# Kernel optimization log

Measured on AMD Instinct MI355X. Metric: run time of the kernel, lower is better.

The kernel has to match this reference:

```python
import jax, jax.numpy as jnp
import numpy as np

N_E, N_W, K = 4096, 8192, 128   # entities, words, factor rank
G, M, J = 1024, 64, 256         # index groups, neighbors per group, entity neighbors
ROW_IND = 17


def setup_inputs() -> dict:
    key = jax.random.key(0)
    ks = jax.random.split(key, 9)
    actual = jax.random.normal(ks[0], (N_E, N_W), dtype=jnp.float32)
    prediction = jax.random.normal(ks[1], (N_E, N_W), dtype=jnp.float32)
    W = jax.random.normal(ks[2], (K, N_W), dtype=jnp.float32)
    E = jax.random.normal(ks[3], (N_E, K), dtype=jnp.float32)
    Sw = jax.random.uniform(ks[4], (N_W, N_W), dtype=jnp.float32)
    Se = jax.random.uniform(ks[5], (N_E, N_E), dtype=jnp.float32)
    word_i_indices = jax.random.randint(ks[6], (G, M), 0, N_W, dtype=jnp.int32)
    entity_j_indices = jax.random.randint(ks[7], (J,), 0, N_E, dtype=jnp.int32)
    sample_j_indices = jax.random.randint(ks[8], (G,), 0, N_W, dtype=jnp.int32)
    return {
        "actual": actual, "prediction": prediction, "W": W, "E": E,
        "Sw": Sw, "Se": Se, "lamb": jnp.ones((), dtype=jnp.float32),
        "row_ind": ROW_IND, "word_i_indices": word_i_indices,
        "entity_j_indices": entity_j_indices, "sample_j_indices": sample_j_indices,
    }


def _l2(x):
    return jnp.sqrt(jnp.sum(x * x))


def reference(actual, prediction, W, E, Sw, Se, lamb, row_ind,
              word_i_indices, entity_j_indices, sample_j_indices):
    # (p > 0) * clamp(p, min=0) == relu(p); 2-norm per parameter, summed
    param_penalty = _l2(jax.nn.relu(W)) + _l2(jax.nn.relu(E))

    # similarity_penalty_Sw: per group j, scalar Frobenius norm of
    # (W[:, j] - W[:, i_inds]) times sum of gathered Sw[j, i_inds]
    Wj = W[:, sample_j_indices]            # [K, G]
    Wi = W[:, word_i_indices]              # [K, G, M]
    d = Wj[:, :, None] - Wi                # [K, G, M]
    diff_w = jnp.sqrt(jnp.sum(d * d, axis=(0, 2)))          # [G]
    Sw_g = Sw[sample_j_indices[:, None], word_i_indices]     # [G, M]
    sim_penalty = jnp.sum(diff_w * jnp.sum(Sw_g, axis=1))

    # similarity_penalty_Se: one scalar norm ||E[i] - E[j_inds]||_F
    de = E[row_ind][None, :] - E[entity_j_indices]            # [J, K]
    diff_e = _l2(de)
    sim_penalty = sim_penalty + diff_e * jnp.sum(Se[row_ind, entity_j_indices])

    recon = _l2(actual - prediction)
    return recon + lamb * param_penalty + sim_penalty
```

## Files before the change

### kernel.cpp

```cpp
#include <hip/hip_runtime.h>
#include <math.h>

#define NE 4096
#define NW 8192
#define KK 128
#define GG 1024
#define MM 64
#define JJ 256


__global__ void k_reduce(const float4* __restrict__ A, const float4* __restrict__ P,
                         const float4* __restrict__ W4, const float4* __restrict__ E4,
                         float* __restrict__ acc) {
    const size_t RQ = (size_t)NE * NW / 4;
    const size_t WQ = (size_t)KK * NW / 4;
    const size_t EQ = (size_t)NE * KK / 4;
    const size_t TOT = RQ + WQ + EQ;

    float r0 = 0.f, r1 = 0.f, r2 = 0.f;
    size_t stride = (size_t)gridDim.x * blockDim.x;
    for (size_t i = (size_t)blockIdx.x * blockDim.x + threadIdx.x; i < TOT; i += stride) {
        if (i < RQ) {
            float4 a = A[i];
            float4 p = P[i];
            float dx = a.x - p.x, dy = a.y - p.y, dz = a.z - p.z, dw = a.w - p.w;
            r0 += dx * dx + dy * dy + dz * dz + dw * dw;
        } else if (i < RQ + WQ) {
            float4 w = W4[i - RQ];
            float x = fmaxf(w.x, 0.f), y = fmaxf(w.y, 0.f);
            float z = fmaxf(w.z, 0.f), u = fmaxf(w.w, 0.f);
            r1 += x * x + y * y + z * z + u * u;
        } else {
            float4 e = E4[i - RQ - WQ];
            float x = fmaxf(e.x, 0.f), y = fmaxf(e.y, 0.f);
            float z = fmaxf(e.z, 0.f), u = fmaxf(e.w, 0.f);
            r2 += x * x + y * y + z * z + u * u;
        }
    }

    #pragma unroll
    for (int off = 32; off > 0; off >>= 1) {
        r0 += __shfl_down(r0, off);
        r1 += __shfl_down(r1, off);
        r2 += __shfl_down(r2, off);
    }
    __shared__ float lds[3][4];
    int lane = threadIdx.x & 63, wid = threadIdx.x >> 6;
    if (lane == 0) { lds[0][wid] = r0; lds[1][wid] = r1; lds[2][wid] = r2; }
    __syncthreads();
    if (threadIdx.x == 0) {
        int nw = blockDim.x >> 6;
        float s0 = 0.f, s1 = 0.f, s2 = 0.f;
        for (int w = 0; w < nw; ++w) { s0 += lds[0][w]; s1 += lds[1][w]; s2 += lds[2][w]; }
        atomicAdd(acc + 0, s0);
        atomicAdd(acc + 1, s1);
        atomicAdd(acc + 2, s2);
    }
}

__global__ void k_sim(const float* __restrict__ W, const float* __restrict__ E,
                      const float* __restrict__ Sw, const float* __restrict__ Se,
                      const int* __restrict__ row_ind,
                      const int* __restrict__ wi, const int* __restrict__ ej,
                      const int* __restrict__ sj,
                      float* __restrict__ acc) {
    __shared__ int wi_s[MM];
    __shared__ float lds[2][2];
    const int t = threadIdx.x;
    const int g = blockIdx.x;

    if (g < GG) {
        const int sjv = sj[g];
        if (t < MM) wi_s[t] = wi[g * MM + t];
        __syncthreads();

        const float* Wk = W + (size_t)t * NW;
        const float wj = Wk[sjv];
        float a = 0.f;
        #pragma unroll 16
        for (int m = 0; m < MM; ++m) {
            float x = Wk[wi_s[m]] - wj;
            a = fmaf(x, x, a);
        }
        float sw = (t < MM) ? Sw[(size_t)sjv * NW + wi_s[t]] : 0.f;

        #pragma unroll
        for (int off = 32; off > 0; off >>= 1) {
            a += __shfl_down(a, off);
            sw += __shfl_down(sw, off);
        }
        int lane = t & 63, wid = t >> 6;
        if (lane == 0) { lds[0][wid] = a; lds[1][wid] = sw; }
        __syncthreads();
        if (t == 0) {
            float at = lds[0][0] + lds[0][1];
            float swt = lds[1][0] + lds[1][1];
            atomicAdd(acc + 3, sqrtf(at) * swt);
        }
    } else {
        const int ri = row_ind[0];
        float a = 0.f;
        for (int i = t; i < JJ * KK; i += 128) {
            int j = i >> 7, k = i & 127;
            float x = E[(size_t)ri * KK + k] - E[(size_t)ej[j] * KK + k];
            a = fmaf(x, x, a);
        }
        float se = 0.f;
        for (int j = t; j < JJ; j += 128) se += Se[(size_t)ri * NE + ej[j]];

        #pragma unroll
        for (int off = 32; off > 0; off >>= 1) {
            a += __shfl_down(a, off);
            se += __shfl_down(se, off);
        }
        int lane = t & 63, wid = t >> 6;
        if (lane == 0) { lds[0][wid] = a; lds[1][wid] = se; }
        __syncthreads();
        if (t == 0) {
            atomicAdd(acc + 3, sqrtf(lds[0][0] + lds[0][1]) * (lds[1][0] + lds[1][1]));
        }
    }
}

__global__ void k_final(const float* __restrict__ acc, const float* __restrict__ lamb,
                        float* __restrict__ out) {
    out[0] = sqrtf(acc[0]) + lamb[0] * (sqrtf(acc[1]) + sqrtf(acc[2])) + acc[3];
}

extern "C" void kernel_launch(void* const* d_in, const int* in_sizes, int n_in,
                              void* d_out, int out_size, void* d_ws, size_t ws_size,
                              hipStream_t stream) {
    const float* actual     = (const float*)d_in[0];
    const float* prediction = (const float*)d_in[1];
    const float* W          = (const float*)d_in[2];
    const float* E          = (const float*)d_in[3];
    const float* Sw         = (const float*)d_in[4];
    const float* Se         = (const float*)d_in[5];
    const float* lamb       = (const float*)d_in[6];
    const int*   row_ind    = (const int*)d_in[7];
    const int*   wi         = (const int*)d_in[8];
    const int*   ej         = (const int*)d_in[9];
    const int*   sj         = (const int*)d_in[10];

    float* acc = (float*)d_ws;
    hipMemsetAsync(acc, 0, 4 * sizeof(float), stream);

    k_reduce<<<2048, 256, 0, stream>>>((const float4*)actual, (const float4*)prediction,
                                       (const float4*)W, (const float4*)E, acc);
    k_sim<<<GG + 1, 128, 0, stream>>>(W, E, Sw, Se, row_ind, wi, ej, sj, acc);
    k_final<<<1, 1, 0, stream>>>(acc, lamb, (float*)d_out);
}
```

Baseline: 687.2 us.

## Fuse reduction, similarity, and finalize kernels into one launch with last-block finalize

Merges the bulk reduction, the similarity-penalty work and the final combine into a single kernel, assigning block ranges to each role. A global atomic counter lets the last finishing block compute the output, which removes two extra launches and lets the small gather work overlap with the bandwidth-bound reduction. The similarity blocks grow to 256 threads, splitting the 64 neighbors into two halves. The threadfence-based completion logic adds ordering risk.

```diff
diff --git a/kernel.cpp b/kernel.cpp
--- a/kernel.cpp
+++ b/kernel.cpp
@@ -8,77 +8,82 @@
 #define MM 64
 #define JJ 256
 
+#define NB_R   2048
+#define NB_TOT (NB_R + GG + 1)
 
-__global__ void k_reduce(const float4* __restrict__ A, const float4* __restrict__ P,
-                         const float4* __restrict__ W4, const float4* __restrict__ E4,
-                         float* __restrict__ acc) {
-    const size_t RQ = (size_t)NE * NW / 4;
-    const size_t WQ = (size_t)KK * NW / 4;
-    const size_t EQ = (size_t)NE * KK / 4;
-    const size_t TOT = RQ + WQ + EQ;
 
-    float r0 = 0.f, r1 = 0.f, r2 = 0.f;
-    size_t stride = (size_t)gridDim.x * blockDim.x;
-    for (size_t i = (size_t)blockIdx.x * blockDim.x + threadIdx.x; i < TOT; i += stride) {
-        if (i < RQ) {
-            float4 a = A[i];
-            float4 p = P[i];
-            float dx = a.x - p.x, dy = a.y - p.y, dz = a.z - p.z, dw = a.w - p.w;
-            r0 += dx * dx + dy * dy + dz * dz + dw * dw;
-        } else if (i < RQ + WQ) {
-            float4 w = W4[i - RQ];
-            float x = fmaxf(w.x, 0.f), y = fmaxf(w.y, 0.f);
-            float z = fmaxf(w.z, 0.f), u = fmaxf(w.w, 0.f);
-            r1 += x * x + y * y + z * z + u * u;
-        } else {
-            float4 e = E4[i - RQ - WQ];
-            float x = fmaxf(e.x, 0.f), y = fmaxf(e.y, 0.f);
-            float z = fmaxf(e.z, 0.f), u = fmaxf(e.w, 0.f);
-            r2 += x * x + y * y + z * z + u * u;
+__global__ __launch_bounds__(256) void k_fused(
+    const float4* __restrict__ A, const float4* __restrict__ P,
+    const float4* __restrict__ W4, const float4* __restrict__ E4,
+    const float* __restrict__ W, const float* __restrict__ E,
+    const float* __restrict__ Sw, const float* __restrict__ Se,
+    const int* __restrict__ row_ind,
+    const int* __restrict__ wi, const int* __restrict__ ej,
+    const int* __restrict__ sj,
+    const float* __restrict__ lamb,
+    float* __restrict__ acc, float* __restrict__ out)
+{
+    __shared__ float lds[3][4];
+    __shared__ int wi_s[MM];
+    const int b = blockIdx.x;
+    const int t = threadIdx.x;
+    const int lane = t & 63, wid = t >> 6;
+
+    if (b < NB_R) {
+        const size_t RQ = (size_t)NE * NW / 4;
+        const size_t WQ = (size_t)KK * NW / 4;
+        const size_t EQ = (size_t)NE * KK / 4;
+        const size_t TOT = RQ + WQ + EQ;
+
+        float r0 = 0.f, r1 = 0.f, r2 = 0.f;
+        const size_t stride = (size_t)NB_R * 256;
+        for (size_t i = (size_t)b * 256 + t; i < TOT; i += stride) {
+            if (i < RQ) {
+                float4 a = A[i];
+                float4 p = P[i];
+                float dx = a.x - p.x, dy = a.y - p.y, dz = a.z - p.z, dw = a.w - p.w;
+                r0 += dx * dx + dy * dy + dz * dz + dw * dw;
+            } else if (i < RQ + WQ) {
+                float4 w = W4[i - RQ];
+                float x = fmaxf(w.x, 0.f), y = fmaxf(w.y, 0.f);
+                float z = fmaxf(w.z, 0.f), u = fmaxf(w.w, 0.f);
+                r1 += x * x + y * y + z * z + u * u;
+            } else {
+                float4 e = E4[i - RQ - WQ];
+                float x = fmaxf(e.x, 0.f), y = fmaxf(e.y, 0.f);
+                float z = fmaxf(e.z, 0.f), u = fmaxf(e.w, 0.f);
+                r2 += x * x + y * y + z * z + u * u;
+            }
         }
-    }
-
-    #pragma unroll
-    for (int off = 32; off > 0; off >>= 1) {
-        r0 += __shfl_down(r0, off);
-        r1 += __shfl_down(r1, off);
-        r2 += __shfl_down(r2, off);
-    }
-    __shared__ float lds[3][4];
-    int lane = threadIdx.x & 63, wid = threadIdx.x >> 6;
-    if (lane == 0) { lds[0][wid] = r0; lds[1][wid] = r1; lds[2][wid] = r2; }
-    __syncthreads();
-    if (threadIdx.x == 0) {
-        int nw = blockDim.x >> 6;
-        float s0 = 0.f, s1 = 0.f, s2 = 0.f;
-        for (int w = 0; w < nw; ++w) { s0 += lds[0][w]; s1 += lds[1][w]; s2 += lds[2][w]; }
-        atomicAdd(acc + 0, s0);
-        atomicAdd(acc + 1, s1);
-        atomicAdd(acc + 2, s2);
-    }
-}
-
-__global__ void k_sim(const float* __restrict__ W, const float* __restrict__ E,
-                      const float* __restrict__ Sw, const float* __restrict__ Se,
-                      const int* __restrict__ row_ind,
-                      const int* __restrict__ wi, const int* __restrict__ ej,
-                      const int* __restrict__ sj,
-                      float* __restrict__ acc) {
-    __shared__ int wi_s[MM];
-    __shared__ float lds[2][2];
-    const int t = threadIdx.x;
-    const int g = blockIdx.x;
-
-    if (g < GG) {
+        #pragma unroll
+        for (int off = 32; off > 0; off >>= 1) {
+            r0 += __shfl_down(r0, off);
+            r1 += __shfl_down(r1, off);
+            r2 += __shfl_down(r2, off);
+        }
+        if (lane == 0) { lds[0][wid] = r0; lds[1][wid] = r1; lds[2][wid] = r2; }
+        __syncthreads();
+        if (t == 0) {
+            float s0 = 0.f, s1 = 0.f, s2 = 0.f;
+            #pragma unroll
+            for (int w = 0; w < 4; ++w) { s0 += lds[0][w]; s1 += lds[1][w]; s2 += lds[2][w]; }
+            atomicAdd(acc + 0, s0);
+            atomicAdd(acc + 1, s1);
+            atomicAdd(acc + 2, s2);
+        }
+    } else if (b < NB_R + GG) {
+        const int g = b - NB_R;
         const int sjv = sj[g];
         if (t < MM) wi_s[t] = wi[g * MM + t];
         __syncthreads();
 
-        const float* Wk = W + (size_t)t * NW;
+        const int k = t & 127;
+        const int half = t >> 7;
+        const float* Wk = W + (size_t)k * NW;
         const float wj = Wk[sjv];
         float a = 0.f;
-        #pragma unroll 16
-        for (int m = 0; m < MM; ++m) {
+        #pragma unroll 8
+        for (int m = half * 32; m < half * 32 + 32; ++m) {
             float x = Wk[wi_s[m]] - wj;
             a = fmaf(x, x, a);
         }
@@ -89,42 +94,49 @@
             a += __shfl_down(a, off);
             sw += __shfl_down(sw, off);
         }
-        int lane = t & 63, wid = t >> 6;
         if (lane == 0) { lds[0][wid] = a; lds[1][wid] = sw; }
         __syncthreads();
         if (t == 0) {
-            float at = lds[0][0] + lds[0][1];
-            float swt = lds[1][0] + lds[1][1];
+            float at  = lds[0][0] + lds[0][1] + lds[0][2] + lds[0][3];
+            float swt = lds[1][0] + lds[1][1] + lds[1][2] + lds[1][3];
             atomicAdd(acc + 3, sqrtf(at) * swt);
         }
     } else {
         const int ri = row_ind[0];
         float a = 0.f;
-        for (int i = t; i < JJ * KK; i += 128) {
+        for (int i = t; i < JJ * KK; i += 256) {
             int j = i >> 7, k = i & 127;
             float x = E[(size_t)ri * KK + k] - E[(size_t)ej[j] * KK + k];
             a = fmaf(x, x, a);
         }
-        float se = 0.f;
-        for (int j = t; j < JJ; j += 128) se += Se[(size_t)ri * NE + ej[j]];
+        float se = (t < JJ) ? Se[(size_t)ri * NE + ej[t]] : 0.f;
 
         #pragma unroll
         for (int off = 32; off > 0; off >>= 1) {
             a += __shfl_down(a, off);
             se += __shfl_down(se, off);
         }
-        int lane = t & 63, wid = t >> 6;
         if (lane == 0) { lds[0][wid] = a; lds[1][wid] = se; }
         __syncthreads();
         if (t == 0) {
-            atomicAdd(acc + 3, sqrtf(lds[0][0] + lds[0][1]) * (lds[1][0] + lds[1][1]));
+            float at = lds[0][0] + lds[0][1] + lds[0][2] + lds[0][3];
+            float st = lds[1][0] + lds[1][1] + lds[1][2] + lds[1][3];
+            atomicAdd(acc + 3, sqrtf(at) * st);
         }
     }
-}
 
-__global__ void k_final(const float* __restrict__ acc, const float* __restrict__ lamb,
-                        float* __restrict__ out) {
-    out[0] = sqrtf(acc[0]) + lamb[0] * (sqrtf(acc[1]) + sqrtf(acc[2])) + acc[3];
+    __threadfence();
+    if (t == 0) {
+        unsigned* cnt = (unsigned*)(acc + 4);
+        unsigned done = atomicAdd(cnt, 1u);
+        if (done == NB_TOT - 1) {
+            float a0 = atomicAdd(acc + 0, 0.f);
+            float a1 = atomicAdd(acc + 1, 0.f);
+            float a2 = atomicAdd(acc + 2, 0.f);
+            float a3 = atomicAdd(acc + 3, 0.f);
+            out[0] = sqrtf(a0) + lamb[0] * (sqrtf(a1) + sqrtf(a2)) + a3;
+        }
+    }
 }
 
 extern "C" void kernel_launch(void* const* d_in, const int* in_sizes, int n_in,
@@ -143,10 +155,11 @@
     const int*   sj         = (const int*)d_in[10];
 
     float* acc = (float*)d_ws;
-    hipMemsetAsync(acc, 0, 4 * sizeof(float), stream);
+    hipMemsetAsync(acc, 0, 8 * sizeof(float), stream);
 
-    k_reduce<<<2048, 256, 0, stream>>>((const float4*)actual, (const float4*)prediction,
-                                       (const float4*)W, (const float4*)E, acc);
-    k_sim<<<GG + 1, 128, 0, stream>>>(W, E, Sw, Se, row_ind, wi, ej, sj, acc);
-    k_final<<<1, 1, 0, stream>>>(acc, lamb, (float*)d_out);
+    k_fused<<<NB_TOT, 256, 0, stream>>>(
+        (const float4*)actual, (const float4*)prediction,
+        (const float4*)W, (const float4*)E,
+        W, E, Sw, Se, row_ind, wi, ej, sj, lamb,
+        acc, (float*)d_out);
 }
```

Result: slower. 985.6 us (+43.4%).
